# Kernel optimization log

Measured on AMD Instinct MI355X. Metric: run time of the kernel, lower is better.

## Reference

```python
import jax, jax.numpy as jnp
import numpy as np

BLOCK = 64
# Standard NF4 codebook (bitsandbytes), 16 quantile-based values in [-1, 1].
NF4_CODEBOOK = jnp.array([
    -1.0, -0.6961928009986877, -0.5250730514526367, -0.39491748809814453,
    -0.28444138169288635, -0.18477343022823334, -0.09105003625154495, 0.0,
    0.07958029955625534, 0.16093020141124725, 0.24611230194568634,
    0.33791524171829224, 0.44070982933044434, 0.5626170039176941,
    0.6848514676094055, 1.0], dtype=jnp.float32)


def dequantize_nf4(codes, absmax, shape):
    # codes: int array of 4-bit indices (unpacked), absmax: one scale per BLOCK.
    vals = NF4_CODEBOOK[codes.reshape(-1)]              # [N]
    vals = vals.reshape(-1, BLOCK) * absmax[:, None]    # blockwise rescale
    return vals.reshape(shape)


def setup_inputs() -> dict:
    key = jax.random.key(0)
    k1, k2, k3, k4, k5 = jax.random.split(key, 5)
    B, S, D_IN, D_OUT = 4, 2048, 4096, 4096
    x = jax.random.normal(k1, (B, S, D_IN), dtype=jnp.float32)
    w_codes = jax.random.randint(k2, (D_OUT, D_IN), 0, 16, dtype=jnp.int32)
    w_absmax = jax.random.uniform(k3, (D_OUT * D_IN // BLOCK,), dtype=jnp.float32)
    b_codes = jax.random.randint(k4, (D_OUT,), 0, 16, dtype=jnp.int32)
    b_absmax = jax.random.uniform(k5, (D_OUT // BLOCK,), dtype=jnp.float32)
    return {"x": x, "w_codes": w_codes, "w_absmax": w_absmax,
            "b_codes": b_codes, "b_absmax": b_absmax}


def reference(x, w_codes, w_absmax, b_codes, b_absmax):
    W = dequantize_nf4(w_codes, w_absmax, w_codes.shape)   # [out, in]
    b = dequantize_nf4(b_codes, b_absmax, b_codes.shape)   # [out]
    # F.linear(x, W, b) = x @ W.T + b
    return jnp.einsum('bsd,od->bso', x, W) + b
```

## Files before the change

kernel.cpp:

```cpp
#include <hip/hip_runtime.h>
#include <stdint.h>

typedef __bf16 bf16_t;
typedef __attribute__((ext_vector_type(8))) __bf16 bf16x8;
typedef __attribute__((ext_vector_type(4))) float f32x4;
typedef __attribute__((ext_vector_type(8))) unsigned short ushort8;
typedef __attribute__((ext_vector_type(4))) int int4v;
typedef __attribute__((ext_vector_type(4))) float float4v;

typedef const void __attribute__((address_space(1)))* gptr_t;
typedef void __attribute__((address_space(3)))* lptr_t;

__constant__ float NF4_CB[16] = {
    -1.0f, -0.6961928009986877f, -0.5250730514526367f, -0.39491748809814453f,
    -0.28444138169288635f, -0.18477343022823334f, -0.09105003625154495f, 0.0f,
    0.07958029955625534f, 0.16093020141124725f, 0.24611230194568634f,
    0.33791524171829224f, 0.44070982933044434f, 0.5626170039176941f,
    0.6848514676094055f, 1.0f};

__device__ __forceinline__ unsigned short f32_to_bf16_rne(float f) {
    unsigned int u = __float_as_uint(f);
    u += 0x7FFFu + ((u >> 16) & 1u);
    return (unsigned short)(u >> 16);
}

__global__ void prep_kernel(const int* __restrict__ w_codes,
                            const float* __restrict__ w_absmax,
                            const float* __restrict__ x,
                            const int* __restrict__ b_codes,
                            const float* __restrict__ b_absmax,
                            unsigned short* __restrict__ outW,
                            unsigned short* __restrict__ outA,
                            float* __restrict__ outBias,
                            long w16, long x16, int nbias, long wb, long xb) {
    __shared__ float cb[16];
    if (threadIdx.x < 16) cb[threadIdx.x] = NF4_CB[threadIdx.x];
    __syncthreads();

    long blk = blockIdx.x;
    if (blk < wb) {
        long t = blk * blockDim.x + threadIdx.x;
        if (t >= w16) return;
        long base = t * 16;
        float am = w_absmax[t >> 2];
        int4v c0 = *(const int4v*)(w_codes + base);
        int4v c1 = *(const int4v*)(w_codes + base + 4);
        int4v c2 = *(const int4v*)(w_codes + base + 8);
        int4v c3 = *(const int4v*)(w_codes + base + 12);
        ushort8 v0, v1;
        v0[0] = f32_to_bf16_rne(cb[c0[0]] * am);
        v0[1] = f32_to_bf16_rne(cb[c0[1]] * am);
        v0[2] = f32_to_bf16_rne(cb[c0[2]] * am);
        v0[3] = f32_to_bf16_rne(cb[c0[3]] * am);
        v0[4] = f32_to_bf16_rne(cb[c1[0]] * am);
        v0[5] = f32_to_bf16_rne(cb[c1[1]] * am);
        v0[6] = f32_to_bf16_rne(cb[c1[2]] * am);
        v0[7] = f32_to_bf16_rne(cb[c1[3]] * am);
        v1[0] = f32_to_bf16_rne(cb[c2[0]] * am);
        v1[1] = f32_to_bf16_rne(cb[c2[1]] * am);
        v1[2] = f32_to_bf16_rne(cb[c2[2]] * am);
        v1[3] = f32_to_bf16_rne(cb[c2[3]] * am);
        v1[4] = f32_to_bf16_rne(cb[c3[0]] * am);
        v1[5] = f32_to_bf16_rne(cb[c3[1]] * am);
        v1[6] = f32_to_bf16_rne(cb[c3[2]] * am);
        v1[7] = f32_to_bf16_rne(cb[c3[3]] * am);
        *(ushort8*)(outW + base) = v0;
        *(ushort8*)(outW + base + 8) = v1;
    } else if (blk < wb + xb) {
        long t = (blk - wb) * blockDim.x + threadIdx.x;
        if (t >= x16) return;
        long base = t * 16;
        float4v f0 = *(const float4v*)(x + base);
        float4v f1 = *(const float4v*)(x + base + 4);
        float4v f2 = *(const float4v*)(x + base + 8);
        float4v f3 = *(const float4v*)(x + base + 12);
        ushort8 v0, v1;
        v0[0] = f32_to_bf16_rne(f0[0]);
        v0[1] = f32_to_bf16_rne(f0[1]);
        v0[2] = f32_to_bf16_rne(f0[2]);
        v0[3] = f32_to_bf16_rne(f0[3]);
        v0[4] = f32_to_bf16_rne(f1[0]);
        v0[5] = f32_to_bf16_rne(f1[1]);
        v0[6] = f32_to_bf16_rne(f1[2]);
        v0[7] = f32_to_bf16_rne(f1[3]);
        v1[0] = f32_to_bf16_rne(f2[0]);
        v1[1] = f32_to_bf16_rne(f2[1]);
        v1[2] = f32_to_bf16_rne(f2[2]);
        v1[3] = f32_to_bf16_rne(f2[3]);
        v1[4] = f32_to_bf16_rne(f3[0]);
        v1[5] = f32_to_bf16_rne(f3[1]);
        v1[6] = f32_to_bf16_rne(f3[2]);
        v1[7] = f32_to_bf16_rne(f3[3]);
        *(ushort8*)(outA + base) = v0;
        *(ushort8*)(outA + base + 8) = v1;
    } else {
        int o = (int)(blk - wb - xb) * blockDim.x + threadIdx.x;
        if (o >= nbias) return;
        outBias[o] = cb[b_codes[o]] * b_absmax[o >> 6];
    }
}

__global__ __launch_bounds__(512) void gemm_bias_kernel_256(
        const bf16_t* __restrict__ A, const bf16_t* __restrict__ B,
        const float* __restrict__ bias, float* __restrict__ C,
        int M, int N, int K) {
    __shared__ __align__(16) bf16_t sAB[24576];

    const int t = threadIdx.x;
    const int lane = t & 63;
    const int wave = t >> 6;
    const int tileM = blockIdx.y * 256;
    const int tileN = blockIdx.x * 128;

    const int rloc = lane >> 3;
    const int jsw  = (lane & 7) ^ rloc;
    const bf16_t* srcp[6];
    bf16_t* dstp[6];
#pragma unroll
    for (int j = 0; j < 6; ++j) {
        int c = wave * 6 + j;
        int isB = (c >= 32);
        int r = (isB ? (c - 32) : c) * 8 + rloc;
        const bf16_t* base = isB ? (B + (size_t)(tileN + r) * K)
                                 : (A + (size_t)(tileM + r) * K);
        srcp[j] = base + jsw * 8;
        dstp[j] = &sAB[c * 512 + lane * 8];
    }

    const int wm = wave >> 1;
    const int wn = wave & 1;
    const int la = lane & 15;
    const int jA = lane >> 4;
    const int jj0 = (jA ^ (lane & 7)) * 8;
    const int aoff = (wm * 64 + la) * 64 + jj0;
    const int boff = 16384 + (wn * 64 + la) * 64 + jj0;

    f32x4 acc[4][4] = {};

    for (int kt = 0; kt < K; kt += 64) {
#pragma unroll
        for (int j = 0; j < 6; ++j) {
            __builtin_amdgcn_global_load_lds((gptr_t)(srcp[j]), (lptr_t)(dstp[j]),
                                             16, 0, 0);
            srcp[j] += 64;
        }
        __syncthreads();

#pragma unroll
        for (int kh = 0; kh < 2; ++kh) {
            const int kx = kh * 32;
            bf16x8 a[4], b[4];
#pragma unroll
            for (int i = 0; i < 4; ++i) a[i] = *(const bf16x8*)&sAB[(aoff + i * 1024) ^ kx];
#pragma unroll
            for (int i = 0; i < 4; ++i) b[i] = *(const bf16x8*)&sAB[(boff + i * 1024) ^ kx];
#pragma unroll
            for (int mi = 0; mi < 4; ++mi)
#pragma unroll
                for (int ni = 0; ni < 4; ++ni)
                    acc[mi][ni] = __builtin_amdgcn_mfma_f32_16x16x32_bf16(
                        a[mi], b[ni], acc[mi][ni], 0, 0, 0);
        }
        __syncthreads();
    }

    const int col0 = tileN + wn * 64 + la;
    const int row0 = tileM + wm * 64 + jA * 4;
    float bv[4];
#pragma unroll
    for (int ni = 0; ni < 4; ++ni) bv[ni] = bias[col0 + ni * 16];
#pragma unroll
    for (int mi = 0; mi < 4; ++mi)
#pragma unroll
        for (int ni = 0; ni < 4; ++ni)
#pragma unroll
            for (int r = 0; r < 4; ++r)
                C[(size_t)(row0 + mi * 16 + r) * N + (col0 + ni * 16)] =
                    acc[mi][ni][r] + bv[ni];
}

__global__ void gemm_bias_kernel_128(const bf16_t* __restrict__ A,
                                     const bf16_t* __restrict__ B,
                                     const float* __restrict__ bias,
                                     float* __restrict__ C,
                                     int M, int N, int K) {
    __shared__ __align__(16) bf16_t sAB[16384];
    const int t = threadIdx.x;
    const int lane = t & 63;
    const int wave = t >> 6;
    const int tileM = blockIdx.y * 128;
    const int tileN = blockIdx.x * 128;

    const int rloc = lane >> 3;
    const int jsw  = (lane & 7) ^ rloc;
    const int chunk0 = wave * 8;
    const int isB = chunk0 >> 4;
    const int ci0 = chunk0 & 15;
    const int r0 = ci0 * 8 + rloc;
    const bf16_t* srcp = (isB ? (B + (size_t)(tileN + r0) * K)
                              : (A + (size_t)(tileM + r0) * K)) + jsw * 8;
    bf16_t* dstp = &sAB[isB * 8192 + ci0 * 512 + lane * 8];
    const size_t srcChunkStride = (size_t)8 * K;

    const int wm = wave >> 1;
    const int wn = wave & 1;
    const int la = lane & 15;
    const int jA = lane >> 4;
    const int jj0 = (jA ^ (lane & 7)) * 8;
    const int aoff = (wm * 64 + la) * 64 + jj0;
    const int boff = 8192 + (wn * 64 + la) * 64 + jj0;

    f32x4 acc[4][4] = {};
    for (int kt = 0; kt < K; kt += 64) {
#pragma unroll
        for (int j8 = 0; j8 < 8; ++j8)
            __builtin_amdgcn_global_load_lds((gptr_t)(srcp + j8 * srcChunkStride),
                                             (lptr_t)(dstp + j8 * 512), 16, 0, 0);
        srcp += 64;
        __syncthreads();
#pragma unroll
        for (int kh = 0; kh < 2; ++kh) {
            const int kx = kh * 32;
            bf16x8 a[4], b[4];
#pragma unroll
            for (int i = 0; i < 4; ++i) a[i] = *(const bf16x8*)&sAB[(aoff + i * 1024) ^ kx];
#pragma unroll
            for (int i = 0; i < 4; ++i) b[i] = *(const bf16x8*)&sAB[(boff + i * 1024) ^ kx];
#pragma unroll
            for (int mi = 0; mi < 4; ++mi)
#pragma unroll
                for (int ni = 0; ni < 4; ++ni)
                    acc[mi][ni] = __builtin_amdgcn_mfma_f32_16x16x32_bf16(
                        a[mi], b[ni], acc[mi][ni], 0, 0, 0);
        }
        __syncthreads();
    }
    const int col0 = tileN + wn * 64 + la;
    const int row0 = tileM + wm * 64 + jA * 4;
    float bv[4];
#pragma unroll
    for (int ni = 0; ni < 4; ++ni) bv[ni] = bias[col0 + ni * 16];
#pragma unroll
    for (int mi = 0; mi < 4; ++mi)
#pragma unroll
        for (int ni = 0; ni < 4; ++ni)
#pragma unroll
            for (int r = 0; r < 4; ++r)
                C[(size_t)(row0 + mi * 16 + r) * N + (col0 + ni * 16)] =
                    acc[mi][ni][r] + bv[ni];
}

extern "C" void kernel_launch(void* const* d_in, const int* in_sizes, int n_in,
                              void* d_out, int out_size, void* d_ws, size_t ws_size,
                              hipStream_t stream) {
    const float* x        = (const float*)d_in[0];
    const int*   w_codes  = (const int*)d_in[1];
    const float* w_absmax = (const float*)d_in[2];
    const int*   b_codes  = (const int*)d_in[3];
    const float* b_absmax = (const float*)d_in[4];
    float* out = (float*)d_out;

    const int  D_OUT = in_sizes[3];
    const long WK    = (long)in_sizes[1];
    const int  D_IN  = (int)(WK / D_OUT);
    const long xN    = (long)in_sizes[0];
    const int  M     = (int)(xN / D_IN);
    const int  N = D_OUT, K = D_IN;

    unsigned short* wsW = (unsigned short*)d_ws;
    unsigned short* wsA = wsW + (size_t)N * K;
    float* wsBias = (float*)(wsA + (size_t)M * K);

    long w16 = WK / 16;
    long x16 = xN / 16;
    long wb = (w16 + 255) / 256;
    long xb = (x16 + 255) / 256;
    long bb = (D_OUT + 255) / 256;
    prep_kernel<<<dim3((unsigned)(wb + xb + bb)), dim3(256), 0, stream>>>(
        w_codes, w_absmax, x, b_codes, b_absmax, wsW, wsA, wsBias,
        w16, x16, D_OUT, wb, xb);

    if (M % 256 == 0) {
        gemm_bias_kernel_256<<<dim3(N / 128, M / 256), dim3(512), 0, stream>>>(
            (const bf16_t*)wsA, (const bf16_t*)wsW, wsBias, out, M, N, K);
    } else {
        gemm_bias_kernel_128<<<dim3(N / 128, M / 128), dim3(256), 0, stream>>>(
            (const bf16_t*)wsA, (const bf16_t*)wsW, wsBias, out, M, N, K);
    }
}
```

Baseline: 504.2 us.

## Add 256x256-tile GEMM kernel with XCD-aware block remap and double-buffered LDS

Adds a new bf16 MFMA GEMM kernel that computes 256x256 output tiles per 512-thread workgroup, replacing the 256x128 tile for the test shape. Each workgroup double-buffers 64-wide K slices into 128KB of LDS using global_load_lds, and remaps block IDs so neighbouring tiles land on the same XCD. The larger tile doubles operand reuse and cuts global/L2 traffic per FLOP. In exchange it raises register pressure (128 accumulators per thread) and LDS use, which limits occupancy to one workgroup per CU.

```diff
diff --git a/kernel.cpp b/kernel.cpp
--- a/kernel.cpp
+++ b/kernel.cpp
@@ -100,6 +100,123 @@
     }
 }
 
+__global__ __launch_bounds__(512, 2) void gemm_bias_kernel_256x256(
+        const bf16_t* __restrict__ A, const bf16_t* __restrict__ B,
+        const float* __restrict__ bias, float* __restrict__ C,
+        int M, int N, int K) {
+    __shared__ __align__(16) bf16_t sAB[65536];
+
+    const int t = threadIdx.x;
+    const int lane = t & 63;
+    const int wave = t >> 6;
+
+    const int nbx = gridDim.x;
+    const int nwg = nbx * (int)gridDim.y;
+    int flat = (int)blockIdx.y * nbx + (int)blockIdx.x;
+    if ((nwg & 7) == 0) flat = (flat & 7) * (nwg >> 3) + (flat >> 3);
+    const int tileM = (flat / nbx) * 256;
+    const int tileN = (flat % nbx) * 256;
+
+    const int rloc = lane >> 3;
+    const int jsw  = (lane & 7) ^ rloc;
+    const bf16_t* srcp[8];
+#pragma unroll
+    for (int j = 0; j < 8; ++j) {
+        int c = wave * 8 + j;
+        int isB = c >> 5;
+        int r = (c & 31) * 8 + rloc;
+        const bf16_t* base = isB ? (B + (size_t)(tileN + r) * K)
+                                 : (A + (size_t)(tileM + r) * K);
+        srcp[j] = base + jsw * 8;
+    }
+    bf16_t* dst0 = &sAB[wave * 4096 + lane * 8];
+
+    auto stage = [&](int bufsel) {
+        bf16_t* d = dst0 + bufsel * 32768;
+#pragma unroll
+        for (int j = 0; j < 8; ++j) {
+            __builtin_amdgcn_global_load_lds((gptr_t)srcp[j],
+                                             (lptr_t)(d + j * 512), 16, 0, 0);
+            srcp[j] += 64;
+        }
+    };
+
+    const int wm = wave >> 2;
+    const int wn = wave & 3;
+    const int la = lane & 15;
+    const int jA = lane >> 4;
+    const int jj0 = (jA ^ (lane & 7)) * 8;
+    const int aoff = (wm * 128 + la) * 64 + jj0;
+    const int boff = 16384 + (wn * 64 + la) * 64 + jj0;
+
+    f32x4 acc[8][4] = {};
+    const int nt = K >> 6;
+
+    stage(0);
+    stage(1);
+    asm volatile("s_waitcnt vmcnt(8)" ::: "memory");
+    __builtin_amdgcn_s_barrier();
+    asm volatile("" ::: "memory");
+
+    for (int kt = 0; kt < nt; ++kt) {
+        const int base = (kt & 1) << 15;
+#pragma unroll
+        for (int kh = 0; kh < 2; ++kh) {
+            const int kx = kh << 5;
+            bf16x8 a[4], b[4];
+#pragma unroll
+            for (int i = 0; i < 4; ++i)
+                b[i] = *(const bf16x8*)&sAB[((boff + i * 1024) ^ kx) + base];
+#pragma unroll
+            for (int i = 0; i < 4; ++i)
+                a[i] = *(const bf16x8*)&sAB[((aoff + i * 1024) ^ kx) + base];
+            __builtin_amdgcn_s_setprio(1);
+#pragma unroll
+            for (int mi = 0; mi < 4; ++mi)
+#pragma unroll
+                for (int ni = 0; ni < 4; ++ni)
+                    acc[mi][ni] = __builtin_amdgcn_mfma_f32_16x16x32_bf16(
+                        a[mi], b[ni], acc[mi][ni], 0, 0, 0);
+            __builtin_amdgcn_s_setprio(0);
+#pragma unroll
+            for (int i = 0; i < 4; ++i)
+                a[i] = *(const bf16x8*)&sAB[((aoff + (i + 4) * 1024) ^ kx) + base];
+            __builtin_amdgcn_s_setprio(1);
+#pragma unroll
+            for (int mi = 0; mi < 4; ++mi)
+#pragma unroll
+                for (int ni = 0; ni < 4; ++ni)
+                    acc[mi + 4][ni] = __builtin_amdgcn_mfma_f32_16x16x32_bf16(
+                        a[mi], b[ni], acc[mi + 4][ni], 0, 0, 0);
+            __builtin_amdgcn_s_setprio(0);
+        }
+        asm volatile("" ::: "memory");
+        __builtin_amdgcn_s_barrier();
+        if (kt + 2 < nt) {
+            stage(kt & 1);
+            asm volatile("s_waitcnt vmcnt(8)" ::: "memory");
+        } else {
+            asm volatile("s_waitcnt vmcnt(0)" ::: "memory");
+        }
+        __builtin_amdgcn_s_barrier();
+        asm volatile("" ::: "memory");
+    }
+
+    const int col0 = tileN + wn * 64 + la;
+    const int row0 = tileM + wm * 128 + jA * 4;
+    float bv[4];
+#pragma unroll
+    for (int ni = 0; ni < 4; ++ni) bv[ni] = bias[col0 + ni * 16];
+#pragma unroll
+    for (int mi = 0; mi < 8; ++mi)
+#pragma unroll
+        for (int ni = 0; ni < 4; ++ni)
+#pragma unroll
+            for (int r = 0; r < 4; ++r)
+                C[(size_t)(row0 + mi * 16 + r) * N + (col0 + ni * 16)] =
+                    acc[mi][ni][r] + bv[ni];
+}
+
 __global__ __launch_bounds__(512) void gemm_bias_kernel_256(
         const bf16_t* __restrict__ A, const bf16_t* __restrict__ B,
         const float* __restrict__ bias, float* __restrict__ C,
@@ -280,7 +397,10 @@
         w_codes, w_absmax, x, b_codes, b_absmax, wsW, wsA, wsBias,
         w16, x16, D_OUT, wb, xb);
 
-    if (M % 256 == 0) {
+    if (M % 256 == 0 && N % 256 == 0 && K % 64 == 0 && K >= 128) {
+        gemm_bias_kernel_256x256<<<dim3(N / 256, M / 256), dim3(512), 0, stream>>>(
+            (const bf16_t*)wsA, (const bf16_t*)wsW, wsBias, out, M, N, K);
+    } else if (M % 256 == 0) {
         gemm_bias_kernel_256<<<dim3(N / 128, M / 256), dim3(512), 0, stream>>>(
             (const bf16_t*)wsA, (const bf16_t*)wsW, wsBias, out, M, N, K);
     } else {
```

Result: slower. 514.5 us (+2.0%).
